# Optimization experiments

Measured on AMD Instinct MI355X. Metric: run time of the kernel, lower is better.

The kernel has to match this reference:

```python
import jax, jax.numpy as jnp
import numpy as np

N = 100000          # nodes
E = 1600000         # edges
D_NODE = 128        # num_node_features
D_EDGE = 128        # num_edge_features
OUT = 64            # out_features
HEADS = 2
HID = OUT * HEADS   # 128
NUM_GRAPHS = 64
NEG_SLOPE = 0.2


def setup_inputs() -> dict:
    key = jax.random.key(0)
    ks = jax.random.split(key, 12)
    glorot = lambda k, shape: jax.random.uniform(
        k, shape, jnp.float32, -1.0, 1.0) * np.sqrt(6.0 / (shape[0] + shape[-1]))
    return {
        "x": jax.random.normal(ks[0], (N, D_NODE), jnp.float32),
        "edge_index": jax.random.randint(ks[1], (2, E), 0, N, jnp.int64),
        "edge_attr": jax.random.normal(ks[2], (E, D_EDGE), jnp.float32),
        "batch": jnp.sort(jax.random.randint(ks[3], (N,), 0, NUM_GRAPHS, jnp.int64)),
        # GATConv params
        "lin_w": glorot(ks[4], (D_NODE, HID)),
        "att_src": glorot(ks[5], (HEADS, OUT)),
        "att_dst": glorot(ks[6], (HEADS, OUT)),
        "gat_bias": jnp.zeros((HID,), jnp.float32),
        # edge_lin params
        "edge_w": glorot(ks[7], (D_EDGE, HID)),
        "edge_b": jnp.zeros((HID,), jnp.float32),
        # MLP params
        "w1": glorot(ks[8], (HID, 32)),
        "b1": jnp.zeros((32,), jnp.float32),
        "w2": glorot(ks[9], (32, 1)),
        "b2": jnp.zeros((1,), jnp.float32),
    }


def reference(x, edge_index, edge_attr, batch, lin_w, att_src, att_dst,
              gat_bias, edge_w, edge_b, w1, b1, w2, b2):
    n = x.shape[0]
    # --- GATConv (concat=True, add_self_loops=True, negative_slope=0.2) ---
    h = (x @ lin_w).reshape(n, HEADS, OUT)                 # [N,H,C]
    loop = jnp.arange(n, dtype=edge_index.dtype)
    src = jnp.concatenate([edge_index[0], loop])           # [E+N]
    dst = jnp.concatenate([edge_index[1], loop])
    a_src = jnp.sum(h * att_src, axis=-1)                  # [N,H]
    a_dst = jnp.sum(h * att_dst, axis=-1)
    e = jax.nn.leaky_relu(a_src[src] + a_dst[dst], NEG_SLOPE)  # [E+N,H]
    e_max = jax.ops.segment_max(e, dst, num_segments=n)    # softmax over incoming edges
    e_exp = jnp.exp(e - e_max[dst])
    denom = jax.ops.segment_sum(e_exp, dst, num_segments=n)
    alpha = e_exp / (denom[dst] + 1e-16)                   # [E+N,H]
    msg = h[src] * alpha[:, :, None]                       # [E+N,H,C]
    node_feat = jax.ops.segment_sum(msg, dst, num_segments=n)
    node_feat = node_feat.reshape(n, HID) + gat_bias       # [N,HID]
    # --- edge features: linear + scatter-add to SOURCE node (the python loop) ---
    edge_feat = edge_attr @ edge_w + edge_b                # [E,HID]
    edge_agg = jax.ops.segment_sum(edge_feat, edge_index[0], num_segments=n)
    combined = node_feat + edge_agg                        # [N,HID]
    # --- global_add_pool + MLP ---
    pooled = jax.ops.segment_sum(combined, batch, num_segments=NUM_GRAPHS)
    return (pooled @ w1 + b1) @ w2 + b2                    # [NUM_GRAPHS,1]
```

## Files before the change

### kernel.cpp

```cpp
#include <hip/hip_runtime.h>
#include <hip/hip_bf16.h>
#include <math.h>


#define NG 64
#define EA_SPLITS 64
#define PH1 40
#define PH2 24

typedef float f32x4 __attribute__((ext_vector_type(4)));

__device__ __forceinline__ float lrelu(float v){ return v > 0.f ? v : 0.2f*v; }

__global__ __launch_bounds__(256) void k_zero(float4* __restrict__ p, long long n4,
                                              int* __restrict__ nstart)
{
  long long i = (long long)blockIdx.x*256 + threadIdx.x;
  long long stride = (long long)gridDim.x*256;
  float4 z = make_float4(0.f,0.f,0.f,0.f);
  for (; i < n4; i += stride) p[i] = z;
  if (blockIdx.x == 0 && threadIdx.x < NG) nstart[threadIdx.x] = 0x7fffffff;
}

__global__ __launch_bounds__(256) void k_deg_nstart(
  const int* __restrict__ src, const int* __restrict__ batch,
  int* __restrict__ deg, int* __restrict__ nstart, int N, int E)
{
  int e = blockIdx.x*256 + threadIdx.x;
  if (e < E) atomicAdd(&deg[src[e]], 1);
  if (e < N){
    int bb = batch[e];
    if (e == 0 || batch[e-1] != bb) atomicMin(&nstart[bb], e);
  }
}

__global__ __launch_bounds__(256) void k_bsum(
  const int* __restrict__ deg, int* __restrict__ bsum, int N)
{
  __shared__ int s[256];
  int b = blockIdx.x, t = threadIdx.x, base = b*1024;
  int sum = 0;
  #pragma unroll
  for (int q=0;q<4;++q){ int i = base + t*4 + q; if (i < N) sum += deg[i]; }
  s[t] = sum; __syncthreads();
  for (int o=128;o;o>>=1){ if (t<o) s[t]+=s[t+o]; __syncthreads(); }
  if (t==0) bsum[b] = s[0];
}

__global__ void k_bscan(const int* __restrict__ bsum, int* __restrict__ boff,
                        int* __restrict__ doff, int nbk, int N, int E)
{
  if (threadIdx.x == 0){
    int s = 0;
    for (int b=0;b<nbk;++b){ boff[b]=s; s+=bsum[b]; }
    doff[N] = E;
  }
}

__global__ __launch_bounds__(256) void k_doff(
  const int* __restrict__ deg, const int* __restrict__ boff,
  int* __restrict__ doff, int* __restrict__ gpos, int N)
{
  __shared__ int s[256];
  int b = blockIdx.x, t = threadIdx.x, base = b*1024;
  int v[4]; int t4 = 0;
  #pragma unroll
  for (int q=0;q<4;++q){ int i = base + t*4 + q; v[q] = (i<N)?deg[i]:0; t4 += v[q]; }
  s[t] = t4; __syncthreads();
  for (int o=1;o<256;o<<=1){
    int add = (t>=o)? s[t-o] : 0;
    __syncthreads();
    s[t] += add;
    __syncthreads();
  }
  int run = boff[b] + s[t] - t4;
  #pragma unroll
  for (int q=0;q<4;++q){
    int i = base + t*4 + q;
    if (i < N){ doff[i] = run; gpos[i] = run; run += v[q]; }
  }
}

__global__ __launch_bounds__(256) void k_scatter(
  const int* __restrict__ src, const int* __restrict__ dst,
  const int* __restrict__ batch, int* __restrict__ gpos,
  int2* __restrict__ order2, const int* __restrict__ nstart,
  const int* __restrict__ doff, int* __restrict__ goff_e,
  float* __restrict__ cnt_nf, float* __restrict__ cnt_ef, int N, int E)
{
  if (blockIdx.x == 0 && threadIdx.x == 0){
    int arr[NG+1];
    arr[NG] = N;
    for (int g=NG-1; g>=0; --g){
      int v = nstart[g];
      arr[g] = (v <= N) ? v : arr[g+1];
    }
    for (int g=0; g<NG; ++g) goff_e[g] = doff[arr[g]];
    goff_e[NG] = E;
    for (int g=0; g<NG; ++g){
      cnt_nf[g] = (float)(arr[g+1]-arr[g]);
      cnt_ef[g] = (float)(goff_e[g+1]-goff_e[g]);
    }
  }
  int e = blockIdx.x*256 + threadIdx.x; if (e >= E) return;
  int s = src[e], d = dst[e];
  int gb = batch[d];
  int p = atomicAdd(&gpos[s], 1);
  order2[p] = make_int2(e, d | ((s & 63) << 17) | (gb << 23));
}

__device__ __forceinline__ void eattr_body(
  int g, int k, const int2* __restrict__ order2,
  const int* __restrict__ goff_e, const float* __restrict__ ea,
  float* __restrict__ pooled_e, int* sord, float* facc, int t)
{
  int start = goff_e[g], cnt = goff_e[g+1] - start;
  int len = (cnt + EA_SPLITS - 1) / EA_SPLITS;
  int i0 = start + k*len;
  int i1 = start + cnt; if (i0 + len < i1) i1 = i0 + len;
  int lane = t & 31, sub = t >> 5;
  const f32x4* ea4 = (const f32x4*)ea;
  f32x4 acc = {0.f,0.f,0.f,0.f};
  for (int base = i0; base < i1; base += 512){
    int m = i1 - base; if (m > 512) m = 512;
    __syncthreads();
    for (int idx = t; idx < m; idx += 256) sord[idx] = order2[base + idx].x;
    __syncthreads();
    int j = sub;
    for (; j + 56 < m; j += 64){
      f32x4 v0 = __builtin_nontemporal_load(&ea4[(size_t)sord[j     ]*32 + lane]);
      f32x4 v1 = __builtin_nontemporal_load(&ea4[(size_t)sord[j +  8]*32 + lane]);
      f32x4 v2 = __builtin_nontemporal_load(&ea4[(size_t)sord[j + 16]*32 + lane]);
      f32x4 v3 = __builtin_nontemporal_load(&ea4[(size_t)sord[j + 24]*32 + lane]);
      f32x4 v4 = __builtin_nontemporal_load(&ea4[(size_t)sord[j + 32]*32 + lane]);
      f32x4 v5 = __builtin_nontemporal_load(&ea4[(size_t)sord[j + 40]*32 + lane]);
      f32x4 v6 = __builtin_nontemporal_load(&ea4[(size_t)sord[j + 48]*32 + lane]);
      f32x4 v7 = __builtin_nontemporal_load(&ea4[(size_t)sord[j + 56]*32 + lane]);
      acc += (v0+v1)+(v2+v3)+((v4+v5)+(v6+v7));
    }
    for (; j < m; j += 8){
      acc += __builtin_nontemporal_load(&ea4[(size_t)sord[j]*32 + lane]);
    }
  }
  __syncthreads();
  if (t < 128) facc[t] = 0.f;
  __syncthreads();
  float* a = &facc[lane*4];
  atomicAdd(a+0, acc.x); atomicAdd(a+1, acc.y);
  atomicAdd(a+2, acc.z); atomicAdd(a+3, acc.w);
  __syncthreads();
  if (t < 128) atomicAdd(&pooled_e[g*128 + t], facc[t]);
}

__global__ __launch_bounds__(256) void k_mega1(
  const float* __restrict__ x, const float* __restrict__ W,
  const float* __restrict__ att_src, const float* __restrict__ att_dst,
  float* __restrict__ h, float* __restrict__ aS, float* __restrict__ aD,
  float* __restrict__ denom,
  const int2* __restrict__ order2, const int* __restrict__ goff_e,
  const float* __restrict__ ea, float* __restrict__ pooled_e,
  int N, int nEA1, int nGH)
{
  __shared__ float lds[32*128];
  int b = blockIdx.x, grp = b/9, rem = b - grp*9;
  int t = threadIdx.x;

  if (rem < 4){
    int eid = grp*4 + rem; if (eid >= nEA1) return;
    eattr_body(eid / PH1, eid % PH1, order2, goff_e, ea, pooled_e,
               (int*)lds, lds + 1024, t);
    return;
  }

  int gid = grp*5 + (rem-4); if (gid >= nGH) return;
  int rb = gid * 32;
  for (int idx = t; idx < 32*128/4; idx += 256){
    int k = (idx*4) & 127;
    int row = rb + (idx >> 5);
    f32x4 v = {0.f,0.f,0.f,0.f};
    if (row < N) v = __builtin_nontemporal_load((const f32x4*)&x[(size_t)row*128 + k]);
    *(f32x4*)&lds[idx*4] = v;
  }
  __syncthreads();
  int ty = t >> 5, tx = t & 31;
  int r0 = ty*4, c0 = tx*4;
  float acc[4][4] = {};
  #pragma unroll 4
  for (int k = 0; k < 128; ++k){
    float4 bv = *(const float4*)&W[k*128 + c0];
    float a0 = lds[(r0+0)*128 + k];
    float a1 = lds[(r0+1)*128 + k];
    float a2 = lds[(r0+2)*128 + k];
    float a3 = lds[(r0+3)*128 + k];
    acc[0][0] += a0*bv.x; acc[0][1] += a0*bv.y; acc[0][2] += a0*bv.z; acc[0][3] += a0*bv.w;
    acc[1][0] += a1*bv.x; acc[1][1] += a1*bv.y; acc[1][2] += a1*bv.z; acc[1][3] += a1*bv.w;
    acc[2][0] += a2*bv.x; acc[2][1] += a2*bv.y; acc[2][2] += a2*bv.z; acc[2][3] += a2*bv.w;
    acc[3][0] += a3*bv.x; acc[3][1] += a3*bv.y; acc[3][2] += a3*bv.z; acc[3][3] += a3*bv.w;
  }
  #pragma unroll
  for (int i=0;i<4;++i){
    int row = rb + r0 + i;
    if (row < N){
      float4 v = make_float4(acc[i][0],acc[i][1],acc[i][2],acc[i][3]);
      *(float4*)&h[(size_t)row*128 + c0] = v;
    }
  }
  float4 vs = *(const float4*)&att_src[c0];
  float4 vd = *(const float4*)&att_dst[c0];
  int head = tx >> 4;
  #pragma unroll
  for (int i=0;i<4;++i){
    float ps = acc[i][0]*vs.x + acc[i][1]*vs.y + acc[i][2]*vs.z + acc[i][3]*vs.w;
    float pd = acc[i][0]*vd.x + acc[i][1]*vd.y + acc[i][2]*vd.z + acc[i][3]*vd.w;
    ps += __shfl_xor(ps,1); ps += __shfl_xor(ps,2); ps += __shfl_xor(ps,4); ps += __shfl_xor(ps,8);
    pd += __shfl_xor(pd,1); pd += __shfl_xor(pd,2); pd += __shfl_xor(pd,4); pd += __shfl_xor(pd,8);
    if ((tx & 15) == 0){
      int row = rb + r0 + i;
      if (row < N){
        aS[row*2+head] = ps;
        aD[row*2+head] = pd;
        denom[row*2+head] = __expf(lrelu(ps+pd));
      }
    }
  }
}

__global__ __launch_bounds__(256) void k_denom(
  const int* __restrict__ src, const int* __restrict__ dst,
  const float* __restrict__ aS, const float* __restrict__ aD,
  float* __restrict__ denom, int E)
{
  int e = blockIdx.x*256 + threadIdx.x; if (e >= E) return;
  int s = src[e], d = dst[e];
  float2 as = *(const float2*)&aS[(size_t)s*2];
  float2 ad = *(const float2*)&aD[(size_t)d*2];
  atomicAdd(&denom[d*2+0], __expf(lrelu(as.x+ad.x)));
  atomicAdd(&denom[d*2+1], __expf(lrelu(as.y+ad.y)));
}

__global__ __launch_bounds__(256) void k_mega2(
  const int2* __restrict__ order2, const int* __restrict__ doff,
  const float* __restrict__ aS, const float* __restrict__ aD,
  const float* __restrict__ denom, const int* __restrict__ batch,
  float* __restrict__ P,
  const float* __restrict__ ea, const int* __restrict__ goff_e,
  float* __restrict__ pooled_e, int N, int nEA2, int nAB)
{
  __shared__ float row[64*128];
  __shared__ float saS[128];
  __shared__ int sb[64];
  int b = blockIdx.x, t = threadIdx.x;

  if (b & 1){
    int eid = b >> 1; if (eid >= nEA2) return;
    eattr_body(eid / PH2, PH1 + eid % PH2, order2, goff_e, ea, pooled_e,
               (int*)row, row + 1024, t);
    return;
  }

  int aid = b >> 1; if (aid >= nAB) return;
  int s0 = aid*64;
  for (int idx=t; idx<2048; idx+=256) ((float4*)row)[idx] = make_float4(0,0,0,0);
  if (t < 128){ int i = s0*2 + t; saS[t] = (i < 2*N) ? aS[i] : 0.f; }
  if (t < 64){ int i = s0 + t; sb[t] = (i < N) ? batch[i] : 0; }
  __syncthreads();
  int hi = s0 + 64; if (hi > N) hi = N;
  int i0 = doff[s0], i1 = doff[hi];
  for (int i = i0 + t; i < i1; i += 256){
    int y = order2[i].y;
    int d = y & 0x1FFFF;
    int lo = (y >> 17) & 63;
    int gb = (y >> 23) & 63;
    float2 ad = *(const float2*)&aD[(size_t)d*2];
    float2 dn = *(const float2*)&denom[(size_t)d*2];
    float a0 = __expf(lrelu(saS[lo*2+0] + ad.x)) / (dn.x + 1e-16f);
    float a1 = __expf(lrelu(saS[lo*2+1] + ad.y)) / (dn.y + 1e-16f);
    atomicAdd(&row[lo*128 + gb],      a0);
    atomicAdd(&row[lo*128 + 64 + gb], a1);
  }
  __syncthreads();
  if (t < 64){
    int s = s0 + t;
    if (s < N){
      float2 ad = *(const float2*)&aD[(size_t)s*2];
      float2 dn = *(const float2*)&denom[(size_t)s*2];
      row[t*128 + sb[t]]      += __expf(lrelu(saS[t*2+0] + ad.x)) / (dn.x + 1e-16f);
      row[t*128 + 64 + sb[t]] += __expf(lrelu(saS[t*2+1] + ad.y)) / (dn.y + 1e-16f);
    }
  }
  __syncthreads();
  for (int idx=t; idx<2048; idx+=256){
    int r = idx >> 5;
    int s = s0 + r;
    if (s < N) ((float4*)&P[(size_t)s*128])[idx & 31] = ((float4*)row)[idx];
  }
}

__global__ __launch_bounds__(256) void k_pgemm(
  const float* __restrict__ P, const float* __restrict__ h,
  float* __restrict__ partial, int N)
{
  __shared__ float sP[64*128];
  int t = threadIdx.x;
  int c = t & 127;
  int gh = t >> 7;
  int head = c >> 6;
  float acc[32];
  #pragma unroll
  for (int i=0;i<32;++i) acc[i] = 0.f;
  int j0 = blockIdx.x * 128;
  for (int sbi=0; sbi<2; ++sbi){
    int jb = j0 + sbi*64;
    __syncthreads();
    for (int idx=t; idx<2048; idx+=256){
      int j = jb + (idx >> 5);
      ((float4*)sP)[idx] = (j < N) ? ((const float4*)&P[(size_t)j*128])[idx & 31]
                                   : make_float4(0,0,0,0);
    }
    __syncthreads();
    for (int jj=0; jj<64; ++jj){
      int j = jb + jj;
      float hv = (j < N) ? h[(size_t)j*128 + c] : 0.f;
      const float* rp = &sP[jj*128 + head*64 + gh*32];
      #pragma unroll
      for (int q=0;q<8;++q){
        float4 pv = *(const float4*)&rp[q*4];
        acc[q*4+0] += pv.x*hv; acc[q*4+1] += pv.y*hv;
        acc[q*4+2] += pv.z*hv; acc[q*4+3] += pv.w*hv;
      }
    }
  }
  float* pb = &partial[(size_t)blockIdx.x*8192];
  #pragma unroll
  for (int i=0;i<32;++i) pb[(gh*32+i)*128 + c] = acc[i];
}

__global__ __launch_bounds__(256) void k_pg_reduce(
  const float* __restrict__ partial, float* __restrict__ pooled_gat, int nPB)
{
  int o = blockIdx.x*256 + threadIdx.x;
  int chunk = (nPB + gridDim.y - 1) / gridDim.y;
  int b0 = blockIdx.y * chunk;
  int b1 = b0 + chunk; if (b1 > nPB) b1 = nPB;
  float s = 0.f;
  for (int b=b0; b<b1; ++b) s += partial[(size_t)b*8192 + o];
  atomicAdd(&pooled_gat[o], s);
}

__global__ __launch_bounds__(128) void k_final(
  const float* __restrict__ pooled_gat, const float* __restrict__ pooled_e,
  const float* __restrict__ cnt_nf, const float* __restrict__ cnt_ef,
  const float* __restrict__ gat_bias, const float* __restrict__ edge_w,
  const float* __restrict__ edge_b, const float* __restrict__ w1,
  const float* __restrict__ b1, const float* __restrict__ w2,
  const float* __restrict__ b2, float* __restrict__ out)
{
  __shared__ float lds_e[128], comb[128], t1[32];
  int g = blockIdx.x, c = threadIdx.x;
  lds_e[c] = pooled_e[g*128 + c];
  __syncthreads();
  float acc = pooled_gat[g*128 + c] + cnt_nf[g]*gat_bias[c] + cnt_ef[g]*edge_b[c];
  for (int k=0; k<128; ++k) acc += lds_e[k] * edge_w[k*128 + c];
  comb[c] = acc;
  __syncthreads();
  if (c < 32){
    float tv = b1[c];
    for (int k=0; k<128; ++k) tv += comb[k] * w1[k*32 + c];
    t1[c] = tv;
  }
  __syncthreads();
  if (c == 0){
    float o = b2[0];
    #pragma unroll
    for (int m=0; m<32; ++m) o += t1[m] * w2[m];
    out[g] = o;
  }
}

extern "C" void kernel_launch(void* const* d_in, const int* in_sizes, int n_in,
                              void* d_out, int out_size, void* d_ws, size_t ws_size,
                              hipStream_t stream) {
  const float* x        = (const float*)d_in[0];
  const int*   ei       = (const int*)d_in[1];
  const float* ea       = (const float*)d_in[2];
  const int*   batch    = (const int*)d_in[3];
  const float* lin_w    = (const float*)d_in[4];
  const float* att_src  = (const float*)d_in[5];
  const float* att_dst  = (const float*)d_in[6];
  const float* gat_bias = (const float*)d_in[7];
  const float* edge_w   = (const float*)d_in[8];
  const float* edge_b   = (const float*)d_in[9];
  const float* w1       = (const float*)d_in[10];
  const float* b1       = (const float*)d_in[11];
  const float* w2       = (const float*)d_in[12];
  const float* b2       = (const float*)d_in[13];
  float* out = (float*)d_out;

  int N = in_sizes[0] / 128;
  int E = in_sizes[1] / 2;
  const int* src = ei;
  const int* dst = ei + E;
  int nbk = (N + 1023) / 1024;
  int nPB = (N + 127) / 128;
  int nAB = (N + 63) / 64;
  int nGH = (N + 31) / 32;
  int nEA1 = NG * PH1;
  int nEA2 = NG * PH2;
  int grp1 = ((nEA1+3)/4 > (nGH+4)/5) ? (nEA1+3)/4 : (nGH+4)/5;
  int grid1 = grp1 * 9;
  int mx2 = (nEA2 > nAB) ? nEA2 : nAB;
  int grid2 = mx2 * 2;

  char* ws = (char*)d_ws;
  size_t off = 0;
  float* pooled_e   = (float*)(ws + off); off += (size_t)NG*128*4;
  float* pooled_gat = (float*)(ws + off); off += (size_t)NG*128*4;
  int*   deg        = (int*)  (ws + off); off += ((size_t)N*4 + 15) & ~15ull;
  size_t zero_bytes = off;
  float* h        = (float*)(ws + off); off += (size_t)N*128*4;
  float* P        = (float*)(ws + off); off += (size_t)N*128*4;
  float* partial  = (float*)(ws + off); off += (size_t)nPB*8192*4;
  float* aS       = (float*)(ws + off); off += (size_t)2*N*4;
  float* aD       = (float*)(ws + off); off += (size_t)2*N*4;
  float* denom    = (float*)(ws + off); off += (size_t)2*N*4;
  int*   doff     = (int*)  (ws + off); off += ((size_t)(N+1)*4 + 15) & ~15ull;
  int*   gpos     = (int*)  (ws + off); off += ((size_t)N*4 + 15) & ~15ull;
  int2*  order2   = (int2*) (ws + off); off += (size_t)E*8;
  int*   bsum     = (int*)  (ws + off); off += 1024*4;
  int*   boff     = (int*)  (ws + off); off += 1024*4;
  int*   nstart   = (int*)  (ws + off); off += NG*4;
  int*   goff_e   = (int*)  (ws + off); off += (NG+1)*4;
  float* cnt_nf   = (float*)(ws + off); off += NG*4;
  float* cnt_ef   = (float*)(ws + off); off += NG*4;

  k_zero<<<128, 256, 0, stream>>>((float4*)d_ws, (long long)(zero_bytes/16), nstart);

  k_deg_nstart<<<(E+255)/256, 256, 0, stream>>>(src, batch, deg, nstart, N, E);
  k_bsum      <<<nbk, 256, 0, stream>>>(deg, bsum, N);
  k_bscan     <<<1, 1, 0, stream>>>(bsum, boff, doff, nbk, N, E);
  k_doff      <<<nbk, 256, 0, stream>>>(deg, boff, doff, gpos, N);
  k_scatter   <<<(E+255)/256, 256, 0, stream>>>(src, dst, batch, gpos, order2,
                                                nstart, doff, goff_e,
                                                cnt_nf, cnt_ef, N, E);

  k_mega1<<<grid1, 256, 0, stream>>>(x, lin_w, att_src, att_dst,
                                     h, aS, aD, denom,
                                     order2, goff_e, ea, pooled_e,
                                     N, nEA1, nGH);

  k_denom<<<(E+255)/256, 256, 0, stream>>>(src, dst, aS, aD, denom, E);

  k_mega2<<<grid2, 256, 0, stream>>>(order2, doff, aS, aD, denom, batch, P,
                                     ea, goff_e, pooled_e, N, nEA2, nAB);

  k_pgemm    <<<nPB, 256, 0, stream>>>(P, h, partial, N);
  {
    dim3 rg(32, 8);
    k_pg_reduce<<<rg, 256, 0, stream>>>(partial, pooled_gat, nPB);
  }

  k_final<<<NG, 128, 0, stream>>>(pooled_gat, pooled_e, cnt_nf, cnt_ef,
                                  gat_bias, edge_w, edge_b, w1, b1, w2, b2, out);
}
```

Measured before the change: 661.9 us.

## Co-schedule scatter with GEMM and denom with edge-attr pooling in merged kernels

Merges the edge scatter into the node-GEMM kernel, because the two are independent, and merges the denominator atomics into a kernel that also runs part of the edge-attribute gather. The remaining edge-attribute splits co-run with the alpha kernel. This removes one launch and overlaps independent work across stages, in place of interleaving block roles within each kernel. Block roles are now contiguous ranges rather than interleaved, which may change load balance, and the edge-attribute work is split 12/52 between the two kernels.

```diff
diff --git a/kernel.cpp b/kernel.cpp
--- a/kernel.cpp
+++ b/kernel.cpp
@@ -5,8 +5,7 @@
 
 #define NG 64
 #define EA_SPLITS 64
-#define PH1 40
-#define PH2 24
+#define KB_SPLIT 12
 
 typedef float f32x4 __attribute__((ext_vector_type(4)));
 
@@ -81,98 +80,44 @@
   }
 }
 
-__global__ __launch_bounds__(256) void k_scatter(
+__global__ __launch_bounds__(256) void k_mega_sg(
   const int* __restrict__ src, const int* __restrict__ dst,
   const int* __restrict__ batch, int* __restrict__ gpos,
   int2* __restrict__ order2, const int* __restrict__ nstart,
   const int* __restrict__ doff, int* __restrict__ goff_e,
-  float* __restrict__ cnt_nf, float* __restrict__ cnt_ef, int N, int E)
-{
-  if (blockIdx.x == 0 && threadIdx.x == 0){
-    int arr[NG+1];
-    arr[NG] = N;
-    for (int g=NG-1; g>=0; --g){
-      int v = nstart[g];
-      arr[g] = (v <= N) ? v : arr[g+1];
-    }
-    for (int g=0; g<NG; ++g) goff_e[g] = doff[arr[g]];
-    goff_e[NG] = E;
-    for (int g=0; g<NG; ++g){
-      cnt_nf[g] = (float)(arr[g+1]-arr[g]);
-      cnt_ef[g] = (float)(goff_e[g+1]-goff_e[g]);
-    }
-  }
-  int e = blockIdx.x*256 + threadIdx.x; if (e >= E) return;
-  int s = src[e], d = dst[e];
-  int gb = batch[d];
-  int p = atomicAdd(&gpos[s], 1);
-  order2[p] = make_int2(e, d | ((s & 63) << 17) | (gb << 23));
-}
-
-__device__ __forceinline__ void eattr_body(
-  int g, int k, const int2* __restrict__ order2,
-  const int* __restrict__ goff_e, const float* __restrict__ ea,
-  float* __restrict__ pooled_e, int* sord, float* facc, int t)
-{
-  int start = goff_e[g], cnt = goff_e[g+1] - start;
-  int len = (cnt + EA_SPLITS - 1) / EA_SPLITS;
-  int i0 = start + k*len;
-  int i1 = start + cnt; if (i0 + len < i1) i1 = i0 + len;
-  int lane = t & 31, sub = t >> 5;
-  const f32x4* ea4 = (const f32x4*)ea;
-  f32x4 acc = {0.f,0.f,0.f,0.f};
-  for (int base = i0; base < i1; base += 512){
-    int m = i1 - base; if (m > 512) m = 512;
-    __syncthreads();
-    for (int idx = t; idx < m; idx += 256) sord[idx] = order2[base + idx].x;
-    __syncthreads();
-    int j = sub;
-    for (; j + 56 < m; j += 64){
-      f32x4 v0 = __builtin_nontemporal_load(&ea4[(size_t)sord[j     ]*32 + lane]);
-      f32x4 v1 = __builtin_nontemporal_load(&ea4[(size_t)sord[j +  8]*32 + lane]);
-      f32x4 v2 = __builtin_nontemporal_load(&ea4[(size_t)sord[j + 16]*32 + lane]);
-      f32x4 v3 = __builtin_nontemporal_load(&ea4[(size_t)sord[j + 24]*32 + lane]);
-      f32x4 v4 = __builtin_nontemporal_load(&ea4[(size_t)sord[j + 32]*32 + lane]);
-      f32x4 v5 = __builtin_nontemporal_load(&ea4[(size_t)sord[j + 40]*32 + lane]);
-      f32x4 v6 = __builtin_nontemporal_load(&ea4[(size_t)sord[j + 48]*32 + lane]);
-      f32x4 v7 = __builtin_nontemporal_load(&ea4[(size_t)sord[j + 56]*32 + lane]);
-      acc += (v0+v1)+(v2+v3)+((v4+v5)+(v6+v7));
-    }
-    for (; j < m; j += 8){
-      acc += __builtin_nontemporal_load(&ea4[(size_t)sord[j]*32 + lane]);
-    }
-  }
-  __syncthreads();
-  if (t < 128) facc[t] = 0.f;
-  __syncthreads();
-  float* a = &facc[lane*4];
-  atomicAdd(a+0, acc.x); atomicAdd(a+1, acc.y);
-  atomicAdd(a+2, acc.z); atomicAdd(a+3, acc.w);
-  __syncthreads();
-  if (t < 128) atomicAdd(&pooled_e[g*128 + t], facc[t]);
-}
-
-__global__ __launch_bounds__(256) void k_mega1(
+  float* __restrict__ cnt_nf, float* __restrict__ cnt_ef,
   const float* __restrict__ x, const float* __restrict__ W,
   const float* __restrict__ att_src, const float* __restrict__ att_dst,
   float* __restrict__ h, float* __restrict__ aS, float* __restrict__ aD,
-  float* __restrict__ denom,
-  const int2* __restrict__ order2, const int* __restrict__ goff_e,
-  const float* __restrict__ ea, float* __restrict__ pooled_e,
-  int N, int nEA1, int nGH)
+  float* __restrict__ denom, int N, int E, int nSC)
 {
   __shared__ float lds[32*128];
-  int b = blockIdx.x, grp = b/9, rem = b - grp*9;
-  int t = threadIdx.x;
-
-  if (rem < 4){
-    int eid = grp*4 + rem; if (eid >= nEA1) return;
-    eattr_body(eid / PH1, eid % PH1, order2, goff_e, ea, pooled_e,
-               (int*)lds, lds + 1024, t);
+  int b = blockIdx.x, t = threadIdx.x;
+
+  if (b < nSC){
+    if (b == 0 && t == 0){
+      int arr[NG+1];
+      arr[NG] = N;
+      for (int g=NG-1; g>=0; --g){
+        int v = nstart[g];
+        arr[g] = (v <= N) ? v : arr[g+1];
+      }
+      for (int g=0; g<NG; ++g) goff_e[g] = doff[arr[g]];
+      goff_e[NG] = E;
+      for (int g=0; g<NG; ++g){
+        cnt_nf[g] = (float)(arr[g+1]-arr[g]);
+        cnt_ef[g] = (float)(goff_e[g+1]-goff_e[g]);
+      }
+    }
+    int e = b*256 + t; if (e >= E) return;
+    int s = src[e], d = dst[e];
+    int gb = batch[d];
+    int p = atomicAdd(&gpos[s], 1);
+    order2[p] = make_int2(e, d | ((s & 63) << 17) | (gb << 23));
     return;
   }
 
-  int gid = grp*5 + (rem-4); if (gid >= nGH) return;
+  int gid = b - nSC;
   int rb = gid * 32;
   for (int idx = t; idx < 32*128/4; idx += 256){
     int k = (idx*4) & 127;
@@ -225,12 +170,65 @@
   }
 }
 
-__global__ __launch_bounds__(256) void k_denom(
+__device__ __forceinline__ void eattr_body(
+  int g, int k, const int2* __restrict__ order2,
+  const int* __restrict__ goff_e, const float* __restrict__ ea,
+  float* __restrict__ pooled_e, int* sord, float* facc, int t)
+{
+  int start = goff_e[g], cnt = goff_e[g+1] - start;
+  int len = (cnt + EA_SPLITS - 1) / EA_SPLITS;
+  int i0 = start + k*len;
+  int i1 = start + cnt; if (i0 + len < i1) i1 = i0 + len;
+  int lane = t & 31, sub = t >> 5;
+  const f32x4* ea4 = (const f32x4*)ea;
+  f32x4 acc = {0.f,0.f,0.f,0.f};
+  for (int base = i0; base < i1; base += 512){
+    int m = i1 - base; if (m > 512) m = 512;
+    __syncthreads();
+    for (int idx = t; idx < m; idx += 256) sord[idx] = order2[base + idx].x;
+    __syncthreads();
+    int j = sub;
+    for (; j + 56 < m; j += 64){
+      f32x4 v0 = __builtin_nontemporal_load(&ea4[(size_t)sord[j     ]*32 + lane]);
+      f32x4 v1 = __builtin_nontemporal_load(&ea4[(size_t)sord[j +  8]*32 + lane]);
+      f32x4 v2 = __builtin_nontemporal_load(&ea4[(size_t)sord[j + 16]*32 + lane]);
+      f32x4 v3 = __builtin_nontemporal_load(&ea4[(size_t)sord[j + 24]*32 + lane]);
+      f32x4 v4 = __builtin_nontemporal_load(&ea4[(size_t)sord[j + 32]*32 + lane]);
+      f32x4 v5 = __builtin_nontemporal_load(&ea4[(size_t)sord[j + 40]*32 + lane]);
+      f32x4 v6 = __builtin_nontemporal_load(&ea4[(size_t)sord[j + 48]*32 + lane]);
+      f32x4 v7 = __builtin_nontemporal_load(&ea4[(size_t)sord[j + 56]*32 + lane]);
+      acc += (v0+v1)+(v2+v3)+((v4+v5)+(v6+v7));
+    }
+    for (; j < m; j += 8){
+      acc += __builtin_nontemporal_load(&ea4[(size_t)sord[j]*32 + lane]);
+    }
+  }
+  __syncthreads();
+  if (t < 128) facc[t] = 0.f;
+  __syncthreads();
+  float* a = &facc[lane*4];
+  atomicAdd(a+0, acc.x); atomicAdd(a+1, acc.y);
+  atomicAdd(a+2, acc.z); atomicAdd(a+3, acc.w);
+  __syncthreads();
+  if (t < 128) atomicAdd(&pooled_e[g*128 + t], facc[t]);
+}
+
+__global__ __launch_bounds__(256) void k_mega_b(
+  const int2* __restrict__ order2, const int* __restrict__ goff_e,
+  const float* __restrict__ ea, float* __restrict__ pooled_e,
   const int* __restrict__ src, const int* __restrict__ dst,
   const float* __restrict__ aS, const float* __restrict__ aD,
-  float* __restrict__ denom, int E)
-{
-  int e = blockIdx.x*256 + threadIdx.x; if (e >= E) return;
+  float* __restrict__ denom, int E, int nEAB)
+{
+  __shared__ int sord[512];
+  __shared__ float facc[128];
+  int b = blockIdx.x, t = threadIdx.x;
+  if (b < nEAB){
+    eattr_body(b / KB_SPLIT, b % KB_SPLIT, order2, goff_e, ea, pooled_e,
+               sord, facc, t);
+    return;
+  }
+  int e = (b - nEAB)*256 + t; if (e >= E) return;
   int s = src[e], d = dst[e];
   float2 as = *(const float2*)&aS[(size_t)s*2];
   float2 ad = *(const float2*)&aD[(size_t)d*2];
@@ -238,27 +236,27 @@
   atomicAdd(&denom[d*2+1], __expf(lrelu(as.y+ad.y)));
 }
 
-__global__ __launch_bounds__(256) void k_mega2(
+__global__ __launch_bounds__(256) void k_mega_c(
   const int2* __restrict__ order2, const int* __restrict__ doff,
   const float* __restrict__ aS, const float* __restrict__ aD,
   const float* __restrict__ denom, const int* __restrict__ batch,
   float* __restrict__ P,
   const float* __restrict__ ea, const int* __restrict__ goff_e,
-  float* __restrict__ pooled_e, int N, int nEA2, int nAB)
+  float* __restrict__ pooled_e, int N, int nEAC)
 {
   __shared__ float row[64*128];
   __shared__ float saS[128];
   __shared__ int sb[64];
   int b = blockIdx.x, t = threadIdx.x;
 
-  if (b & 1){
-    int eid = b >> 1; if (eid >= nEA2) return;
-    eattr_body(eid / PH2, PH1 + eid % PH2, order2, goff_e, ea, pooled_e,
+  if (b < nEAC){
+    const int PHC = EA_SPLITS - KB_SPLIT;
+    eattr_body(b / PHC, KB_SPLIT + b % PHC, order2, goff_e, ea, pooled_e,
                (int*)row, row + 1024, t);
     return;
   }
 
-  int aid = b >> 1; if (aid >= nAB) return;
+  int aid = b - nEAC;
   int s0 = aid*64;
   for (int idx=t; idx<2048; idx+=256) ((float4*)row)[idx] = make_float4(0,0,0,0);
   if (t < 128){ int i = s0*2 + t; saS[t] = (i < 2*N) ? aS[i] : 0.f; }
@@ -404,12 +402,9 @@
   int nPB = (N + 127) / 128;
   int nAB = (N + 63) / 64;
   int nGH = (N + 31) / 32;
-  int nEA1 = NG * PH1;
-  int nEA2 = NG * PH2;
-  int grp1 = ((nEA1+3)/4 > (nGH+4)/5) ? (nEA1+3)/4 : (nGH+4)/5;
-  int grid1 = grp1 * 9;
-  int mx2 = (nEA2 > nAB) ? nEA2 : nAB;
-  int grid2 = mx2 * 2;
+  int nSC = (E + 255) / 256;
+  int nEAB = NG * KB_SPLIT;
+  int nEAC = NG * (EA_SPLITS - KB_SPLIT);
 
   char* ws = (char*)d_ws;
   size_t off = 0;
@@ -439,19 +434,17 @@
   k_bsum      <<<nbk, 256, 0, stream>>>(deg, bsum, N);
   k_bscan     <<<1, 1, 0, stream>>>(bsum, boff, doff, nbk, N, E);
   k_doff      <<<nbk, 256, 0, stream>>>(deg, boff, doff, gpos, N);
-  k_scatter   <<<(E+255)/256, 256, 0, stream>>>(src, dst, batch, gpos, order2,
-                                                nstart, doff, goff_e,
-                                                cnt_nf, cnt_ef, N, E);
-
-  k_mega1<<<grid1, 256, 0, stream>>>(x, lin_w, att_src, att_dst,
-                                     h, aS, aD, denom,
-                                     order2, goff_e, ea, pooled_e,
-                                     N, nEA1, nGH);
-
-  k_denom<<<(E+255)/256, 256, 0, stream>>>(src, dst, aS, aD, denom, E);
-
-  k_mega2<<<grid2, 256, 0, stream>>>(order2, doff, aS, aD, denom, batch, P,
-                                     ea, goff_e, pooled_e, N, nEA2, nAB);
+
+  k_mega_sg<<<nSC + nGH, 256, 0, stream>>>(src, dst, batch, gpos, order2,
+                                           nstart, doff, goff_e, cnt_nf, cnt_ef,
+                                           x, lin_w, att_src, att_dst,
+                                           h, aS, aD, denom, N, E, nSC);
+
+  k_mega_b<<<nEAB + nSC, 256, 0, stream>>>(order2, goff_e, ea, pooled_e,
+                                           src, dst, aS, aD, denom, E, nEAB);
+
+  k_mega_c<<<nEAC + nAB, 256, 0, stream>>>(order2, doff, aS, aD, denom, batch,
+                                           P, ea, goff_e, pooled_e, N, nEAC);
 
   k_pgemm    <<<nPB, 256, 0, stream>>>(P, h, partial, N);
   {
```

Result: no change. 659.9 us (-0.3%).
